# Performance work log

Measured on AMD Instinct MI355X. Metric: run time of the kernel, lower is better.

The kernel has to match this reference:

```python
import jax, jax.numpy as jnp
import numpy as np

B, C, H = 2, 256, 64
INTER = 64


def setup_inputs() -> dict:
    key = jax.random.key(0)
    ks = jax.random.split(key, 10)
    scale = 1.0 / np.sqrt(C)
    x = jax.random.normal(ks[0], (B, C, H, H), dtype=jnp.float32)
    # binary hole mask (1 = foreground/hole region)
    mask = jnp.round(jax.random.uniform(ks[1], (B, 1, H, H), dtype=jnp.float32))
    def w(k, shape, s):
        return jax.random.normal(k, shape, dtype=jnp.float32) * s
    return {
        "x": x,
        "mask": mask,
        "w_theta_s": w(ks[2], (INTER, C), scale),
        "w_phi_s": w(ks[3], (INTER, C), scale),
        "w_gate_s": w(ks[4], (INTER, C), scale),
        "w_theta_c": w(ks[5], (INTER, C), scale),
        "w_phi_c": w(ks[6], (INTER, C), scale),
        "w_gate_c": w(ks[7], (INTER, C), scale),
        "w_out": w(ks[8], (C, INTER), 1.0 / np.sqrt(INTER)),
    }


def _nonlocal_branch(q_src, kv_src, w_theta, w_phi, w_gate):
    # q_src, kv_src: [B, C, N]; weights: [inter, C]
    K = jnp.einsum('oc,bcn->bon', w_theta, kv_src)   # [B, inter, N]
    Q = jnp.einsum('oc,bcn->bon', w_phi, q_src)      # [B, inter, N]
    score = jnp.einsum('bom,bon->bmn', Q, K)         # [B, Nq, Nk]
    score = jax.nn.softmax(score, axis=-1)
    V = jnp.einsum('oc,bcn->bon', w_gate, kv_src)    # [B, inter, N]
    feat = jnp.einsum('bon,bmn->bom', V, score)      # [B, inter, Nq]
    return feat, score


def reference(x, mask, w_theta_s, w_phi_s, w_gate_s,
              w_theta_c, w_phi_c, w_gate_c, w_out):
    b, c, h = x.shape[0], x.shape[1], x.shape[2]
    n = h * h
    fg = (x * mask).reshape(b, c, n)          # foreground tokens
    bg = (x * (1.0 - mask)).reshape(b, c, n)  # background tokens
    feat_self, score_self = _nonlocal_branch(fg, fg, w_theta_s, w_phi_s, w_gate_s)
    feat_cross, score_cross = _nonlocal_branch(fg, bg, w_theta_c, w_phi_c, w_gate_c)
    fused = jnp.einsum('co,bon->bcn', w_out, feat_self + feat_cross)
    feat = x + fused.reshape(b, c, h, h)
    return feat, score_self, score_cross
```

## Files before the change

### kernel.cpp

```cpp
#include <hip/hip_runtime.h>
#include <hip/hip_bf16.h>
#include <stdint.h>

#define NBATCH 2
#define NCH    256
#define NTOK   4096
#define NINT   64
#define NGRP   4
#define BMROWS 64
#define BNCOLS 128
#define GRPN   (NTOK/NGRP)
#define NCHUNK (GRPN/BNCOLS)

typedef float  f32x4  __attribute__((ext_vector_type(4)));
typedef __bf16 bf16x8 __attribute__((ext_vector_type(8)));
union U16x8 { uint4 u; bf16x8 b; };

#define SZBF      ((size_t)NTOK*NINT)
#define BF_TOTAL  ((size_t)NBATCH*10*SZBF*2)
#define PMAX_OFF  (BF_TOTAL)
#define PSUM_OFF  (PMAX_OFF + (size_t)NBATCH*2*NGRP*NTOK*4)
#define FEAT_OFF  (PSUM_OFF + (size_t)NBATCH*2*NGRP*NTOK*4)

#define OUT_SELF  ((size_t)2097152)
#define OUT_CROSS ((size_t)35651584)

__device__ inline unsigned short f2bf(float x){
  unsigned int u = __builtin_bit_cast(unsigned int, x);
  u = (u + 0x7FFFu + ((u>>16)&1u)) >> 16;
  return (unsigned short)u;
}
__device__ inline float bf2f(unsigned short s){
  unsigned int u = ((unsigned int)s)<<16;
  return __builtin_bit_cast(float, u);
}

typedef __attribute__((address_space(3))) unsigned int lds_u32_t;
typedef __attribute__((address_space(1))) const unsigned int gbl_u32_t;
__device__ inline void async16(const void* g, void* l){
  __builtin_amdgcn_global_load_lds((gbl_u32_t*)g, (lds_u32_t*)l, 16, 0, 0);
}

__global__ __launch_bounds__(256) void k_proj(
    const float* __restrict__ x, const float* __restrict__ mask,
    const float* __restrict__ wts, const float* __restrict__ wps,
    const float* __restrict__ wgs, const float* __restrict__ wtc,
    const float* __restrict__ wpc, const float* __restrict__ wgc,
    char* __restrict__ ws)
{
  int nt = blockIdx.x;
  int j  = blockIdx.y;
  int b  = blockIdx.z;
  const float* W; int isBg, mode, arrH, arrL;
  switch (j) {
    case 0: W=wts; isBg=0; mode=0; arrH=2; arrL=3; break;
    case 1: W=wps; isBg=0; mode=0; arrH=0; arrL=1; break;
    case 2: W=wgs; isBg=0; mode=1; arrH=8; arrL=8; break;
    case 3: W=wpc; isBg=0; mode=0; arrH=4; arrL=5; break;
    case 4: W=wtc; isBg=1; mode=0; arrH=6; arrL=7; break;
    default:W=wgc; isBg=1; mode=1; arrH=9; arrL=9; break;
  }
  __shared__ float xm[256*64];
  __shared__ float msk[64];
  int t = threadIdx.x;
  if (t < 64) {
    float m = mask[(size_t)b*NTOK + nt*64 + t];
    msk[t] = isBg ? (1.0f - m) : m;
  }
  __syncthreads();
  const float* xb = x + (size_t)b*NCH*NTOK + nt*64;
  for (int it = 0; it < 64; ++it) {
    int flat = it*256 + t; int c = flat>>6, nl = flat&63;
    xm[flat] = xb[(size_t)c*NTOK + nl] * msk[nl];
  }
  __syncthreads();
  int nl = t & 63;
  int o0 = __builtin_amdgcn_readfirstlane((t>>6)*16);
  const float* Wr = W + (size_t)o0*256;
  float acc[16];
  #pragma unroll
  for (int i=0;i<16;i++) acc[i]=0.0f;
  #pragma unroll 4
  for (int c=0;c<256;c++){
    float xv = xm[c*64+nl];
    #pragma unroll
    for (int i=0;i<16;i++) acc[i] += Wr[i*256 + c] * xv;
  }
  int n = nt*64 + nl;
  if (mode==0){
    unsigned short* Ah = (unsigned short*)ws + ((size_t)b*10 + arrH)*SZBF;
    unsigned short* Al = (unsigned short*)ws + ((size_t)b*10 + arrL)*SZBF;
    #pragma unroll
    for (int i=0;i<16;i++){
      float v = acc[i];
      unsigned short h = f2bf(v);
      float r = v - bf2f(h);
      Ah[(size_t)n*NINT + o0+i] = h;
      Al[(size_t)n*NINT + o0+i] = f2bf(r);
    }
  } else {
    unsigned short* V = (unsigned short*)ws + ((size_t)b*10 + arrH)*SZBF;
    #pragma unroll
    for (int i=0;i<16;i++) V[(size_t)(o0+i)*NTOK + n] = f2bf(acc[i]);
  }
}

__device__ inline void stage_ktile(const unsigned short* gH, const unsigned short* gL,
                                   unsigned short* lKh, unsigned short* lKl, int t)
{
  #pragma unroll
  for (int it=0; it<4; ++it){
    int f = it*256 + t;
    int r = f >> 3, g = f & 7;
    int gs = g ^ (r & 7);
    size_t goff = (size_t)r*64 + gs*8;
    async16(gH + goff, lKh + (size_t)f*8);
    async16(gL + goff, lKl + (size_t)f*8);
  }
}

__device__ inline void decode_blk(int blk, int& mb, int& ng, int& bbr){
  int xcd  = blk & 7;
  int slot = blk >> 3;
  int combo = xcd*2 + (slot >> 6);
  mb  = slot & 63;
  bbr = combo >> 2;
  ng  = combo & 3;
}

__global__ __launch_bounds__(256) void k_passA(char* __restrict__ ws)
{
  int mb, ng, bbr;
  decode_blk(blockIdx.x, mb, ng, bbr);
  int b = bbr>>1, br = bbr&1;
  const unsigned short* Qh = (const unsigned short*)ws + ((size_t)b*10 + (br?4:0))*SZBF;
  const unsigned short* Ql = Qh + SZBF;
  const unsigned short* Kh = (const unsigned short*)ws + ((size_t)b*10 + (br?6:2))*SZBF;
  const unsigned short* Kl = Kh + SZBF;
  __shared__ __align__(16) unsigned short lKh[BNCOLS*NINT];
  __shared__ __align__(16) unsigned short lKl[BNCOLS*NINT];
  int t = threadIdx.x, lane = t&63, wv = t>>6;
  int m0 = mb*BMROWS + wv*16;
  int rowb = lane&15;
  int mrow = m0 + rowb;
  int q4 = lane>>4;
  int ko = q4*8;
  U16x8 qh[2], ql[2];
  #pragma unroll
  for (int kk=0;kk<2;kk++){
    qh[kk].u = *(const uint4*)(Qh + (size_t)mrow*NINT + kk*32 + ko);
    ql[kk].u = *(const uint4*)(Ql + (size_t)mrow*NINT + kk*32 + ko);
  }
  float M = -3.0e38f, L = 0.0f;
  for (int ch=0; ch<NCHUNK; ++ch){
    int n0 = ng*GRPN + ch*BNCOLS;
    __syncthreads();
    stage_ktile(Kh + (size_t)n0*NINT, Kl + (size_t)n0*NINT, lKh, lKl, t);
    asm volatile("s_waitcnt vmcnt(0)" ::: "memory");
    __syncthreads();
    f32x4 st[8];
    #pragma unroll
    for (int t8=0;t8<8;t8++){
      int row = t8*16 + rowb;
      f32x4 s = {0.0f,0.0f,0.0f,0.0f};
      #pragma unroll
      for (int kk=0;kk<2;kk++){
        int soff = row*64 + (((kk*4 + q4) ^ (row&7))*8);
        U16x8 ah, al;
        ah.u = *(const uint4*)(lKh + soff);
        al.u = *(const uint4*)(lKl + soff);
        s = __builtin_amdgcn_mfma_f32_16x16x32_bf16(ah.b, qh[kk].b, s, 0,0,0);
        s = __builtin_amdgcn_mfma_f32_16x16x32_bf16(ah.b, ql[kk].b, s, 0,0,0);
        s = __builtin_amdgcn_mfma_f32_16x16x32_bf16(al.b, qh[kk].b, s, 0,0,0);
      }
      st[t8] = s;
    }
    float cmax = -3.0e38f;
    #pragma unroll
    for (int t8=0;t8<8;t8++){
      cmax = fmaxf(cmax, fmaxf(fmaxf(st[t8][0],st[t8][1]), fmaxf(st[t8][2],st[t8][3])));
    }
    float newM = fmaxf(M, cmax);
    float s1 = 0.0f;
    #pragma unroll
    for (int t8=0;t8<8;t8++){
      s1 += __expf(st[t8][0]-newM) + __expf(st[t8][1]-newM)
          + __expf(st[t8][2]-newM) + __expf(st[t8][3]-newM);
    }
    L = L*__expf(M-newM) + s1;
    M = newM;
  }
  #pragma unroll
  for (int d=16; d<64; d<<=1){
    float M2 = __shfl_xor(M, d, 64);
    float L2 = __shfl_xor(L, d, 64);
    float nM = fmaxf(M, M2);
    L = L*__expf(M-nM) + L2*__expf(M2-nM);
    M = nM;
  }
  if (q4==0){
    float* pmax = (float*)(ws + PMAX_OFF);
    float* psum = (float*)(ws + PSUM_OFF);
    int idx = (bbr*NGRP + ng)*NTOK + m0 + rowb;
    pmax[idx]=M; psum[idx]=L;
  }
}

__global__ __launch_bounds__(256) void k_passB(char* __restrict__ ws, float* __restrict__ out)
{
  int mb, ng, bbr;
  decode_blk(blockIdx.x, mb, ng, bbr);
  int b = bbr>>1, br = bbr&1;
  const unsigned short* Qh = (const unsigned short*)ws + ((size_t)b*10 + (br?4:0))*SZBF;
  const unsigned short* Ql = Qh + SZBF;
  const unsigned short* Kh = (const unsigned short*)ws + ((size_t)b*10 + (br?6:2))*SZBF;
  const unsigned short* Kl = Kh + SZBF;
  const unsigned short* Vv = (const unsigned short*)ws + ((size_t)b*10 + (br?9:8))*SZBF;
  const float* pmax = (const float*)(ws + PMAX_OFF);
  const float* psum = (const float*)(ws + PSUM_OFF);
  __shared__ __align__(16) unsigned short lKh[BNCOLS*NINT];
  __shared__ __align__(16) unsigned short lKl[BNCOLS*NINT];
  __shared__ __align__(16) unsigned short lP[4][16*136];
  int t = threadIdx.x, lane = t&63, wv = t>>6;
  int m0 = mb*BMROWS + wv*16;
  int rowb = lane&15;
  int mrow = m0 + rowb;
  int q4 = lane>>4;
  int ko = q4*8;
  U16x8 qh[2], ql[2];
  #pragma unroll
  for (int kk=0;kk<2;kk++){
    qh[kk].u = *(const uint4*)(Qh + (size_t)mrow*NINT + kk*32 + ko);
    ql[kk].u = *(const uint4*)(Ql + (size_t)mrow*NINT + kk*32 + ko);
  }
  float Mlane = -3.0e38f;
  #pragma unroll
  for (int g2=0; g2<NGRP; ++g2) Mlane = fmaxf(Mlane, pmax[(bbr*NGRP+g2)*NTOK + mrow]);
  float Lsum = 0.0f;
  #pragma unroll
  for (int g2=0; g2<NGRP; ++g2)
    Lsum += psum[(bbr*NGRP+g2)*NTOK + mrow] * __expf(pmax[(bbr*NGRP+g2)*NTOK + mrow] - Mlane);
  float rL = 1.0f / Lsum;
  float* outS = out + (br ? OUT_CROSS : OUT_SELF) + (size_t)b*NTOK*NTOK;
  f32x4 fac[4];
  #pragma unroll
  for (int ot=0;ot<4;ot++) fac[ot] = (f32x4){0.0f,0.0f,0.0f,0.0f};

  for (int ch=0; ch<NCHUNK; ++ch){
    int n0 = ng*GRPN + ch*BNCOLS;
    __syncthreads();
    stage_ktile(Kh + (size_t)n0*NINT, Kl + (size_t)n0*NINT, lKh, lKl, t);
    asm volatile("s_waitcnt vmcnt(0)" ::: "memory");
    __syncthreads();
    #pragma unroll
    for (int t8=0;t8<8;t8++){
      int row = t8*16 + rowb;
      f32x4 s = {0.0f,0.0f,0.0f,0.0f};
      #pragma unroll
      for (int kk=0;kk<2;kk++){
        int soff = row*64 + (((kk*4 + q4) ^ (row&7))*8);
        U16x8 ah, al;
        ah.u = *(const uint4*)(lKh + soff);
        al.u = *(const uint4*)(lKl + soff);
        s = __builtin_amdgcn_mfma_f32_16x16x32_bf16(ah.b, qh[kk].b, s, 0,0,0);
        s = __builtin_amdgcn_mfma_f32_16x16x32_bf16(ah.b, ql[kk].b, s, 0,0,0);
        s = __builtin_amdgcn_mfma_f32_16x16x32_bf16(al.b, qh[kk].b, s, 0,0,0);
      }
      f32x4 p;
      p[0] = __expf(s[0]-Mlane)*rL;
      p[1] = __expf(s[1]-Mlane)*rL;
      p[2] = __expf(s[2]-Mlane)*rL;
      p[3] = __expf(s[3]-Mlane)*rL;
      int ngl = n0 + t8*16 + q4*4;
      *(f32x4*)(outS + (size_t)mrow*NTOK + ngl) = p;
      unsigned int lo = (unsigned int)f2bf(p[0]) | ((unsigned int)f2bf(p[1])<<16);
      unsigned int hi = (unsigned int)f2bf(p[2]) | ((unsigned int)f2bf(p[3])<<16);
      uint2 pk; pk.x = lo; pk.y = hi;
      *(uint2*)(&lP[wv][rowb*136 + t8*16 + q4*4]) = pk;
    }
    asm volatile("s_waitcnt lgkmcnt(0)" ::: "memory");
    #pragma unroll
    for (int kk4=0; kk4<4; ++kk4){
      U16x8 pa;
      pa.u = *(const uint4*)(&lP[wv][rowb*136 + kk4*32 + ko]);
      #pragma unroll
      for (int ot=0; ot<4; ++ot){
        U16x8 vb;
        vb.u = *(const uint4*)(Vv + (size_t)(ot*16+rowb)*NTOK + n0 + kk4*32 + ko);
        fac[ot] = __builtin_amdgcn_mfma_f32_16x16x32_bf16(pa.b, vb.b, fac[ot], 0,0,0);
      }
    }
    asm volatile("s_waitcnt lgkmcnt(0)" ::: "memory");
  }
  float* feat = (float*)(ws + FEAT_OFF) + ((size_t)(ng*4 + bbr)*NTOK)*NINT;
  #pragma unroll
  for (int ot=0; ot<4; ++ot){
    #pragma unroll
    for (int r=0; r<4; ++r){
      int m = m0 + q4*4 + r;
      feat[(size_t)m*NINT + ot*16 + rowb] = fac[ot][r];
    }
  }
}

__global__ __launch_bounds__(256) void k_epi(
    const float* __restrict__ x, const float* __restrict__ wout,
    const char* __restrict__ ws, float* __restrict__ out)
{
  int nt = blockIdx.x, b = blockIdx.y;
  int t = threadIdx.x, nl = t&63;
  const float* feat = (const float*)(ws + FEAT_OFF);
  __shared__ float fs[64][65];
  for (int it=0; it<16; ++it){
    int flat = it*256 + t; int n_l = flat>>6, o = flat&63;
    float acc = 0.0f;
    #pragma unroll
    for (int ng=0; ng<NGRP; ++ng){
      size_t base = ((size_t)(ng*4 + b*2)*NTOK + nt*64 + n_l)*NINT + o;
      acc += feat[base] + feat[base + (size_t)NTOK*NINT];
    }
    fs[n_l][o] = acc;
  }
  __syncthreads();
  float f[64];
  #pragma unroll
  for (int o=0;o<64;o++) f[o] = fs[nl][o];
  int c0 = __builtin_amdgcn_readfirstlane((t>>6)*64);
  const float* wr = wout + (size_t)c0*64;
  for (int cc=0; cc<64; ++cc){
    int c = c0 + cc;
    float acc = x[((size_t)b*NCH + c)*NTOK + nt*64 + nl];
    #pragma unroll
    for (int o=0;o<64;o++) acc += wr[cc*64+o]*f[o];
    out[((size_t)b*NCH + c)*NTOK + nt*64 + nl] = acc;
  }
}

extern "C" void kernel_launch(void* const* d_in, const int* in_sizes, int n_in,
                              void* d_out, int out_size, void* d_ws, size_t ws_size,
                              hipStream_t stream)
{
  const float* x    = (const float*)d_in[0];
  const float* mask = (const float*)d_in[1];
  const float* wts  = (const float*)d_in[2];
  const float* wps  = (const float*)d_in[3];
  const float* wgs  = (const float*)d_in[4];
  const float* wtc  = (const float*)d_in[5];
  const float* wpc  = (const float*)d_in[6];
  const float* wgc  = (const float*)d_in[7];
  const float* wout = (const float*)d_in[8];
  float* out = (float*)d_out;
  char*  ws  = (char*)d_ws;
  (void)in_sizes; (void)n_in; (void)out_size; (void)ws_size;

  k_proj   <<<dim3(64,6,NBATCH), 256, 0, stream>>>(x, mask, wts, wps, wgs, wtc, wpc, wgc, ws);
  k_passA  <<<dim3(1024), 256, 0, stream>>>(ws);
  k_passB  <<<dim3(1024), 256, 0, stream>>>(ws, out);
  k_epi    <<<dim3(64,NBATCH), 256, 0, stream>>>(x, wout, ws, out);
}
```

Baseline: 567.6 us.

## Fuse two-pass softmax attention into one kernel with unnormalized accumulation

Replaces the separate max/sum pass and score/PV pass with a single kernel. Each block covers 64 query rows and splits the keys across two halves of 512 threads. The first sweep computes exp(score) without max subtraction, accumulating the row sum and the unnormalized P·V together. The second sweep recomputes the scores and writes normalized probabilities with nontemporal stores. It also double-buffers the K tiles in LDS, removes the per-group pmax/psum and feat partials, and simplifies the epilogue reduction. In exchange it drops the max stabilization, so large scores could overflow, and it launches fewer, larger blocks.

After: 559.0 us. No clear change (-1.5%).

```diff
diff --git a/kernel.cpp b/kernel.cpp
--- a/kernel.cpp
+++ b/kernel.cpp
@@ -6,11 +6,8 @@
 #define NCH    256
 #define NTOK   4096
 #define NINT   64
-#define NGRP   4
-#define BMROWS 64
-#define BNCOLS 128
-#define GRPN   (NTOK/NGRP)
-#define NCHUNK (GRPN/BNCOLS)
+#define CHW    64
+#define NCH2   (2048/CHW)
 
 typedef float  f32x4  __attribute__((ext_vector_type(4)));
 typedef __bf16 bf16x8 __attribute__((ext_vector_type(8)));
@@ -18,9 +15,7 @@
 
 #define SZBF      ((size_t)NTOK*NINT)
 #define BF_TOTAL  ((size_t)NBATCH*10*SZBF*2)
-#define PMAX_OFF  (BF_TOTAL)
-#define PSUM_OFF  (PMAX_OFF + (size_t)NBATCH*2*NGRP*NTOK*4)
-#define FEAT_OFF  (PSUM_OFF + (size_t)NBATCH*2*NGRP*NTOK*4)
+#define FEAT_OFF  (BF_TOTAL)
 
 #define OUT_SELF  ((size_t)2097152)
 #define OUT_CROSS ((size_t)35651584)
@@ -105,201 +100,164 @@
   }
 }
 
-__device__ inline void stage_ktile(const unsigned short* gH, const unsigned short* gL,
-                                   unsigned short* lKh, unsigned short* lKl, int t)
+__global__ __launch_bounds__(512) void k_attn(char* __restrict__ ws, float* __restrict__ out)
 {
-  #pragma unroll
-  for (int it=0; it<4; ++it){
-    int f = it*256 + t;
-    int r = f >> 3, g = f & 7;
-    int gs = g ^ (r & 7);
-    size_t goff = (size_t)r*64 + gs*8;
-    async16(gH + goff, lKh + (size_t)f*8);
-    async16(gL + goff, lKl + (size_t)f*8);
-  }
-}
-
-__device__ inline void decode_blk(int blk, int& mb, int& ng, int& bbr){
-  int xcd  = blk & 7;
-  int slot = blk >> 3;
-  int combo = xcd*2 + (slot >> 6);
-  mb  = slot & 63;
-  bbr = combo >> 2;
-  ng  = combo & 3;
-}
-
-__global__ __launch_bounds__(256) void k_passA(char* __restrict__ ws)
-{
-  int mb, ng, bbr;
-  decode_blk(blockIdx.x, mb, ng, bbr);
-  int b = bbr>>1, br = bbr&1;
-  const unsigned short* Qh = (const unsigned short*)ws + ((size_t)b*10 + (br?4:0))*SZBF;
-  const unsigned short* Ql = Qh + SZBF;
-  const unsigned short* Kh = (const unsigned short*)ws + ((size_t)b*10 + (br?6:2))*SZBF;
-  const unsigned short* Kl = Kh + SZBF;
-  __shared__ __align__(16) unsigned short lKh[BNCOLS*NINT];
-  __shared__ __align__(16) unsigned short lKl[BNCOLS*NINT];
-  int t = threadIdx.x, lane = t&63, wv = t>>6;
-  int m0 = mb*BMROWS + wv*16;
-  int rowb = lane&15;
-  int mrow = m0 + rowb;
-  int q4 = lane>>4;
-  int ko = q4*8;
-  U16x8 qh[2], ql[2];
-  #pragma unroll
-  for (int kk=0;kk<2;kk++){
-    qh[kk].u = *(const uint4*)(Qh + (size_t)mrow*NINT + kk*32 + ko);
-    ql[kk].u = *(const uint4*)(Ql + (size_t)mrow*NINT + kk*32 + ko);
-  }
-  float M = -3.0e38f, L = 0.0f;
-  for (int ch=0; ch<NCHUNK; ++ch){
-    int n0 = ng*GRPN + ch*BNCOLS;
-    __syncthreads();
-    stage_ktile(Kh + (size_t)n0*NINT, Kl + (size_t)n0*NINT, lKh, lKl, t);
-    asm volatile("s_waitcnt vmcnt(0)" ::: "memory");
-    __syncthreads();
-    f32x4 st[8];
-    #pragma unroll
-    for (int t8=0;t8<8;t8++){
-      int row = t8*16 + rowb;
-      f32x4 s = {0.0f,0.0f,0.0f,0.0f};
-      #pragma unroll
-      for (int kk=0;kk<2;kk++){
-        int soff = row*64 + (((kk*4 + q4) ^ (row&7))*8);
-        U16x8 ah, al;
-        ah.u = *(const uint4*)(lKh + soff);
-        al.u = *(const uint4*)(lKl + soff);
-        s = __builtin_amdgcn_mfma_f32_16x16x32_bf16(ah.b, qh[kk].b, s, 0,0,0);
-        s = __builtin_amdgcn_mfma_f32_16x16x32_bf16(ah.b, ql[kk].b, s, 0,0,0);
-        s = __builtin_amdgcn_mfma_f32_16x16x32_bf16(al.b, qh[kk].b, s, 0,0,0);
-      }
-      st[t8] = s;
-    }
-    float cmax = -3.0e38f;
-    #pragma unroll
-    for (int t8=0;t8<8;t8++){
-      cmax = fmaxf(cmax, fmaxf(fmaxf(st[t8][0],st[t8][1]), fmaxf(st[t8][2],st[t8][3])));
-    }
-    float newM = fmaxf(M, cmax);
-    float s1 = 0.0f;
-    #pragma unroll
-    for (int t8=0;t8<8;t8++){
-      s1 += __expf(st[t8][0]-newM) + __expf(st[t8][1]-newM)
-          + __expf(st[t8][2]-newM) + __expf(st[t8][3]-newM);
-    }
-    L = L*__expf(M-newM) + s1;
-    M = newM;
-  }
-  #pragma unroll
-  for (int d=16; d<64; d<<=1){
-    float M2 = __shfl_xor(M, d, 64);
-    float L2 = __shfl_xor(L, d, 64);
-    float nM = fmaxf(M, M2);
-    L = L*__expf(M-nM) + L2*__expf(M2-nM);
-    M = nM;
-  }
-  if (q4==0){
-    float* pmax = (float*)(ws + PMAX_OFF);
-    float* psum = (float*)(ws + PSUM_OFF);
-    int idx = (bbr*NGRP + ng)*NTOK + m0 + rowb;
-    pmax[idx]=M; psum[idx]=L;
-  }
-}
-
-__global__ __launch_bounds__(256) void k_passB(char* __restrict__ ws, float* __restrict__ out)
-{
-  int mb, ng, bbr;
-  decode_blk(blockIdx.x, mb, ng, bbr);
-  int b = bbr>>1, br = bbr&1;
+  __shared__ __align__(16) char smem[84480];
+
+  int blk = blockIdx.x;
+  int xcd = blk & 7, idx = blk >> 3;
+  int bbr = xcd >> 1;
+  int mb  = ((xcd & 1) << 5) + idx;
+  int b = bbr >> 1, br = bbr & 1;
   const unsigned short* Qh = (const unsigned short*)ws + ((size_t)b*10 + (br?4:0))*SZBF;
   const unsigned short* Ql = Qh + SZBF;
   const unsigned short* Kh = (const unsigned short*)ws + ((size_t)b*10 + (br?6:2))*SZBF;
   const unsigned short* Kl = Kh + SZBF;
   const unsigned short* Vv = (const unsigned short*)ws + ((size_t)b*10 + (br?9:8))*SZBF;
-  const float* pmax = (const float*)(ws + PMAX_OFF);
-  const float* psum = (const float*)(ws + PSUM_OFF);
-  __shared__ __align__(16) unsigned short lKh[BNCOLS*NINT];
-  __shared__ __align__(16) unsigned short lKl[BNCOLS*NINT];
-  __shared__ __align__(16) unsigned short lP[4][16*136];
-  int t = threadIdx.x, lane = t&63, wv = t>>6;
-  int m0 = mb*BMROWS + wv*16;
-  int rowb = lane&15;
-  int mrow = m0 + rowb;
-  int q4 = lane>>4;
-  int ko = q4*8;
+
+  int t = threadIdx.x, lane = t&63, w = t>>6;
+  int mt = w&3, half = w>>2;
+  int rowb = lane&15, q4 = lane>>4, ko = q4*8;
+  int m0 = mb*64 + mt*16, mrow = m0 + rowb;
+  int th = t & 255;
+
+  unsigned short* lPw = (unsigned short*)(smem + 65536 + w*2304);
+  float* Lb = (float*)(smem + 83968);
+  float* fb = (float*)(smem + 65536);
+
   U16x8 qh[2], ql[2];
   #pragma unroll
   for (int kk=0;kk<2;kk++){
     qh[kk].u = *(const uint4*)(Qh + (size_t)mrow*NINT + kk*32 + ko);
     ql[kk].u = *(const uint4*)(Ql + (size_t)mrow*NINT + kk*32 + ko);
   }
-  float Mlane = -3.0e38f;
-  #pragma unroll
-  for (int g2=0; g2<NGRP; ++g2) Mlane = fmaxf(Mlane, pmax[(bbr*NGRP+g2)*NTOK + mrow]);
-  float Lsum = 0.0f;
-  #pragma unroll
-  for (int g2=0; g2<NGRP; ++g2)
-    Lsum += psum[(bbr*NGRP+g2)*NTOK + mrow] * __expf(pmax[(bbr*NGRP+g2)*NTOK + mrow] - Mlane);
-  float rL = 1.0f / Lsum;
+
+  auto lkbase = [&](int buf)->unsigned short*{
+    return (unsigned short*)(smem + (size_t)(half*2+buf)*16384);
+  };
+  auto stage = [&](int ch, int buf){
+    int n0 = half*2048 + ch*CHW;
+    const unsigned short* gH = Kh + (size_t)n0*NINT;
+    const unsigned short* gL = Kl + (size_t)n0*NINT;
+    unsigned short* LB = lkbase(buf);
+    #pragma unroll
+    for (int it=0; it<2; ++it){
+      int f = it*256 + th;
+      int r = f>>3, g = f&7, gs = g ^ (r&7);
+      size_t goff = (size_t)r*64 + gs*8;
+      async16(gH + goff, LB + (size_t)f*8);
+      async16(gL + goff, LB + 4096 + (size_t)f*8);
+    }
+  };
+
   float* outS = out + (br ? OUT_CROSS : OUT_SELF) + (size_t)b*NTOK*NTOK;
   f32x4 fac[4];
   #pragma unroll
   for (int ot=0;ot<4;ot++) fac[ot] = (f32x4){0.0f,0.0f,0.0f,0.0f};
-
-  for (int ch=0; ch<NCHUNK; ++ch){
-    int n0 = ng*GRPN + ch*BNCOLS;
-    __syncthreads();
-    stage_ktile(Kh + (size_t)n0*NINT, Kl + (size_t)n0*NINT, lKh, lKl, t);
+  float Lacc = 0.0f;
+
+  stage(0, 0);
+  for (int ch=0; ch<NCH2; ++ch){
+    int cur = ch & 1;
     asm volatile("s_waitcnt vmcnt(0)" ::: "memory");
     __syncthreads();
-    #pragma unroll
-    for (int t8=0;t8<8;t8++){
+    if (ch+1 < NCH2) stage(ch+1, cur^1);
+    unsigned short* LB = lkbase(cur);
+    int n0 = half*2048 + ch*CHW;
+    #pragma unroll
+    for (int t8=0; t8<4; ++t8){
       int row = t8*16 + rowb;
       f32x4 s = {0.0f,0.0f,0.0f,0.0f};
       #pragma unroll
-      for (int kk=0;kk<2;kk++){
+      for (int kk=0; kk<2; ++kk){
         int soff = row*64 + (((kk*4 + q4) ^ (row&7))*8);
         U16x8 ah, al;
-        ah.u = *(const uint4*)(lKh + soff);
-        al.u = *(const uint4*)(lKl + soff);
+        ah.u = *(const uint4*)(LB + soff);
+        al.u = *(const uint4*)(LB + 4096 + soff);
+        s = __builtin_amdgcn_mfma_f32_16x16x32_bf16(ah.b, qh[kk].b, s, 0,0,0);
+        s = __builtin_amdgcn_mfma_f32_16x16x32_bf16(ah.b, ql[kk].b, s, 0,0,0);
+        s = __builtin_amdgcn_mfma_f32_16x16x32_bf16(al.b, qh[kk].b, s, 0,0,0);
+      }
+      float p0=__expf(s[0]), p1=__expf(s[1]), p2=__expf(s[2]), p3=__expf(s[3]);
+      Lacc += (p0+p1)+(p2+p3);
+      unsigned int lo = (unsigned int)f2bf(p0) | ((unsigned int)f2bf(p1)<<16);
+      unsigned int hi = (unsigned int)f2bf(p2) | ((unsigned int)f2bf(p3)<<16);
+      uint2 pk; pk.x = lo; pk.y = hi;
+      *(uint2*)(lPw + rowb*72 + t8*16 + q4*4) = pk;
+    }
+    asm volatile("s_waitcnt lgkmcnt(0)" ::: "memory");
+    #pragma unroll
+    for (int kk4=0; kk4<2; ++kk4){
+      U16x8 pa;
+      pa.u = *(const uint4*)(lPw + rowb*72 + kk4*32 + ko);
+      #pragma unroll
+      for (int ot=0; ot<4; ++ot){
+        U16x8 vb;
+        vb.u = *(const uint4*)(Vv + (size_t)(ot*16+rowb)*NTOK + n0 + kk4*32 + ko);
+        fac[ot] = __builtin_amdgcn_mfma_f32_16x16x32_bf16(pa.b, vb.b, fac[ot], 0,0,0);
+      }
+    }
+    asm volatile("s_waitcnt lgkmcnt(0)" ::: "memory");
+    __syncthreads();
+  }
+
+  #pragma unroll
+  for (int d=16; d<64; d<<=1) Lacc += __shfl_xor(Lacc, d, 64);
+  if (q4==0) Lb[w*16 + rowb] = Lacc;
+  __syncthreads();
+
+  if (half==1){
+    #pragma unroll
+    for (int ot=0; ot<4; ++ot)
+      #pragma unroll
+      for (int r=0; r<4; ++r)
+        fb[mt*1024 + (q4*4+r)*64 + ot*16 + rowb] = fac[ot][r];
+  }
+  __syncthreads();
+  if (half==0){
+    float* feat = (float*)(ws + FEAT_OFF) + (size_t)bbr*NTOK*NINT;
+    #pragma unroll
+    for (int r=0; r<4; ++r){
+      int m = q4*4 + r;
+      float rLr = 1.0f / (Lb[mt*16 + m] + Lb[(4+mt)*16 + m]);
+      #pragma unroll
+      for (int ot=0; ot<4; ++ot)
+        feat[(size_t)(m0+m)*NINT + ot*16 + rowb] =
+            (fac[ot][r] + fb[mt*1024 + m*64 + ot*16 + rowb]) * rLr;
+    }
+  }
+  float rLp = 1.0f / (Lb[mt*16 + rowb] + Lb[(4+mt)*16 + rowb]);
+  __syncthreads();
+
+  stage(0, 0);
+  for (int ch=0; ch<NCH2; ++ch){
+    int cur = ch & 1;
+    asm volatile("s_waitcnt vmcnt(0)" ::: "memory");
+    __syncthreads();
+    if (ch+1 < NCH2) stage(ch+1, cur^1);
+    unsigned short* LB = lkbase(cur);
+    int n0 = half*2048 + ch*CHW;
+    #pragma unroll
+    for (int t8=0; t8<4; ++t8){
+      int row = t8*16 + rowb;
+      f32x4 s = {0.0f,0.0f,0.0f,0.0f};
+      #pragma unroll
+      for (int kk=0; kk<2; ++kk){
+        int soff = row*64 + (((kk*4 + q4) ^ (row&7))*8);
+        U16x8 ah, al;
+        ah.u = *(const uint4*)(LB + soff);
+        al.u = *(const uint4*)(LB + 4096 + soff);
         s = __builtin_amdgcn_mfma_f32_16x16x32_bf16(ah.b, qh[kk].b, s, 0,0,0);
         s = __builtin_amdgcn_mfma_f32_16x16x32_bf16(ah.b, ql[kk].b, s, 0,0,0);
         s = __builtin_amdgcn_mfma_f32_16x16x32_bf16(al.b, qh[kk].b, s, 0,0,0);
       }
       f32x4 p;
-      p[0] = __expf(s[0]-Mlane)*rL;
-      p[1] = __expf(s[1]-Mlane)*rL;
-      p[2] = __expf(s[2]-Mlane)*rL;
-      p[3] = __expf(s[3]-Mlane)*rL;
-      int ngl = n0 + t8*16 + q4*4;
-      *(f32x4*)(outS + (size_t)mrow*NTOK + ngl) = p;
-      unsigned int lo = (unsigned int)f2bf(p[0]) | ((unsigned int)f2bf(p[1])<<16);
-      unsigned int hi = (unsigned int)f2bf(p[2]) | ((unsigned int)f2bf(p[3])<<16);
-      uint2 pk; pk.x = lo; pk.y = hi;
-      *(uint2*)(&lP[wv][rowb*136 + t8*16 + q4*4]) = pk;
-    }
-    asm volatile("s_waitcnt lgkmcnt(0)" ::: "memory");
-    #pragma unroll
-    for (int kk4=0; kk4<4; ++kk4){
-      U16x8 pa;
-      pa.u = *(const uint4*)(&lP[wv][rowb*136 + kk4*32 + ko]);
-      #pragma unroll
-      for (int ot=0; ot<4; ++ot){
-        U16x8 vb;
-        vb.u = *(const uint4*)(Vv + (size_t)(ot*16+rowb)*NTOK + n0 + kk4*32 + ko);
-        fac[ot] = __builtin_amdgcn_mfma_f32_16x16x32_bf16(pa.b, vb.b, fac[ot], 0,0,0);
-      }
-    }
-    asm volatile("s_waitcnt lgkmcnt(0)" ::: "memory");
-  }
-  float* feat = (float*)(ws + FEAT_OFF) + ((size_t)(ng*4 + bbr)*NTOK)*NINT;
-  #pragma unroll
-  for (int ot=0; ot<4; ++ot){
-    #pragma unroll
-    for (int r=0; r<4; ++r){
-      int m = m0 + q4*4 + r;
-      feat[(size_t)m*NINT + ot*16 + rowb] = fac[ot][r];
-    }
+      p[0] = __expf(s[0])*rLp; p[1] = __expf(s[1])*rLp;
+      p[2] = __expf(s[2])*rLp; p[3] = __expf(s[3])*rLp;
+      __builtin_nontemporal_store(p,
+          (f32x4*)(outS + (size_t)mrow*NTOK + n0 + t8*16 + q4*4));
+    }
+    __syncthreads();
   }
 }
 
@@ -313,13 +271,9 @@
   __shared__ float fs[64][65];
   for (int it=0; it<16; ++it){
     int flat = it*256 + t; int n_l = flat>>6, o = flat&63;
-    float acc = 0.0f;
-    #pragma unroll
-    for (int ng=0; ng<NGRP; ++ng){
-      size_t base = ((size_t)(ng*4 + b*2)*NTOK + nt*64 + n_l)*NINT + o;
-      acc += feat[base] + feat[base + (size_t)NTOK*NINT];
-    }
-    fs[n_l][o] = acc;
+    size_t r0 = ((size_t)(b*2+0)*NTOK + nt*64 + n_l)*NINT + o;
+    size_t r1 = ((size_t)(b*2+1)*NTOK + nt*64 + n_l)*NINT + o;
+    fs[n_l][o] = feat[r0] + feat[r1];
   }
   __syncthreads();
   float f[64];
@@ -353,8 +307,7 @@
   char*  ws  = (char*)d_ws;
   (void)in_sizes; (void)n_in; (void)out_size; (void)ws_size;
 
-  k_proj   <<<dim3(64,6,NBATCH), 256, 0, stream>>>(x, mask, wts, wps, wgs, wtc, wpc, wgc, ws);
-  k_passA  <<<dim3(1024), 256, 0, stream>>>(ws);
-  k_passB  <<<dim3(1024), 256, 0, stream>>>(ws, out);
-  k_epi    <<<dim3(64,NBATCH), 256, 0, stream>>>(x, wout, ws, out);
-}
+  k_proj <<<dim3(64,6,NBATCH), 256, 0, stream>>>(x, mask, wts, wps, wgs, wtc, wpc, wgc, ws);
+  k_attn <<<dim3(256), 512, 0, stream>>>(ws, out);
+  k_epi  <<<dim3(64,NBATCH), 256, 0, stream>>>(x, wout, ws, out);
+}
```
